# Optimization experiments

Measured on AMD Instinct MI355X. Metric: run time of the kernel, lower is better.

The kernel has to match this reference:

```python
import jax, jax.numpy as jnp
import numpy as np

GROUPS = 32
EPS = 1e-5


def group_norm(x, gamma, beta):
    # x: [B, C, H, W]; normalize over (C//G, H, W) within each of G groups
    B, C, H, W = x.shape
    xg = x.reshape(B, GROUPS, C // GROUPS, H, W)
    mean = xg.mean(axis=(2, 3, 4), keepdims=True)
    var = xg.var(axis=(2, 3, 4), keepdims=True)
    xg = (xg - mean) * jax.lax.rsqrt(var + EPS)
    x = xg.reshape(B, C, H, W)
    return x * gamma[None, :, None, None] + beta[None, :, None, None]


def conv1x1(x, W, b):
    # 1x1 conv == pointwise linear over channels. x: [B,C,H,W], W: [Cout,Cin]
    return jnp.einsum('oc,bchw->bohw', W, x) + b[None, :, None, None]


def setup_inputs() -> dict:
    key = jax.random.key(0)
    ks = jax.random.split(key, 6)
    B, C, H, W = 16, 512, 32, 32
    scale = 1.0 / np.sqrt(C)  # ~kaiming-ish init for 1x1 convs
    return {
        'x': jax.random.normal(ks[0], (B, C, H, W), jnp.float32),
        'gn_gamma': jnp.ones((C,), jnp.float32),
        'gn_beta': jnp.zeros((C,), jnp.float32),
        'Wq': jax.random.normal(ks[1], (C, C), jnp.float32) * scale,
        'bq': jnp.zeros((C,), jnp.float32),
        'Wk': jax.random.normal(ks[2], (C, C), jnp.float32) * scale,
        'bk': jnp.zeros((C,), jnp.float32),
        'Wv': jax.random.normal(ks[3], (C, C), jnp.float32) * scale,
        'bv': jnp.zeros((C,), jnp.float32),
        'Wp': jax.random.normal(ks[4], (C, C), jnp.float32) * scale,
        'bp': jnp.zeros((C,), jnp.float32),
    }


def reference(x, gn_gamma, gn_beta, Wq, bq, Wk, bk, Wv, bv, Wp, bp):
    B, C, H, W = x.shape
    h = group_norm(x, gn_gamma, gn_beta)
    q = conv1x1(h, Wq, bq).reshape(B, C, H * W)  # [B,C,T]
    k = conv1x1(h, Wk, bk).reshape(B, C, H * W)
    v = conv1x1(h, Wv, bv).reshape(B, C, H * W)
    # scores [B, T(query), S(key)] = q^T k, scaled by C^{-1/2}
    w = jnp.einsum('bct,bcs->bts', q, k) * (C ** -0.5)
    w = jax.nn.softmax(w, axis=-1)
    h = jnp.einsum('bts,bcs->bct', w, v).reshape(B, C, H, W)
    h = conv1x1(h, Wp, bp)
    return x + h
```

## Files before the change

kernel.cpp:

```cpp
#include <hip/hip_runtime.h>

typedef unsigned short u16;
typedef __bf16 bf16x8 __attribute__((ext_vector_type(8)));
typedef float f32x4 __attribute__((ext_vector_type(4)));

__device__ __forceinline__ u16 f2bf(float f) {
    unsigned u = __builtin_bit_cast(unsigned, f);
    u += 0x7fffu + ((u >> 16) & 1u);
    return (u16)(u >> 16);
}

#define GLDS16(g, l) __builtin_amdgcn_global_load_lds( \
    (const __attribute__((address_space(1))) void*)(g), \
    (__attribute__((address_space(3))) void*)(l), 16, 0, 0)

#define QK_SCALE 0.044194173824159216f

__global__ __launch_bounds__(256) void convert_kernel(
    const float* __restrict__ Wq, const float* __restrict__ Wk,
    const float* __restrict__ Wv, const float* __restrict__ Wp,
    const float* __restrict__ bq, const float* __restrict__ bk,
    const float* __restrict__ bv,
    u16* __restrict__ Wqkv, u16* __restrict__ Wpb, float* __restrict__ bqkv)
{
    int idx = blockIdx.x * 256 + threadIdx.x;
    if (idx < 786432) {
        int which = idx >> 18;
        int off   = idx & 262143;
        if (which == 0)
            Wqkv[idx] = f2bf(Wq[off] * QK_SCALE);
        else
            Wqkv[idx] = f2bf(((which == 1) ? Wk : Wv)[off]);
    } else {
        int off = idx - 786432;
        Wpb[off] = f2bf(Wp[off]);
    }
    if (idx < 1536) {
        float bvv = (idx < 512) ? bq[idx] * QK_SCALE
                  : (idx < 1024) ? bk[idx & 511] : bv[idx & 511];
        bqkv[idx] = bvv;
    }
}

__global__ __launch_bounds__(256) void gn_stats(
    const float* __restrict__ x, float2* __restrict__ stats)
{
    const int g = blockIdx.x, b = blockIdx.y, tid = threadIdx.x;
    const float* xg = x + ((size_t)b * 512 + (size_t)g * 16) * 1024;

    float s = 0.f, s2 = 0.f;
    const float4* x4 = (const float4*)xg;
    #pragma unroll 4
    for (int i = tid; i < 4096; i += 256) {
        float4 v = x4[i];
        s  += v.x + v.y + v.z + v.w;
        s2 += v.x * v.x + v.y * v.y + v.z * v.z + v.w * v.w;
    }
    #pragma unroll
    for (int off = 32; off; off >>= 1) {
        s  += __shfl_down(s, off);
        s2 += __shfl_down(s2, off);
    }
    __shared__ float rs[4], rs2[4];
    const int w = tid >> 6;
    if ((tid & 63) == 0) { rs[w] = s; rs2[w] = s2; }
    __syncthreads();
    if (tid == 0) {
        float S  = rs[0] + rs[1] + rs[2] + rs[3];
        float S2 = rs2[0] + rs2[1] + rs2[2] + rs2[3];
        float mean = S * (1.f / 16384.f);
        float var  = S2 * (1.f / 16384.f) - mean * mean;
        stats[b * 32 + g] = make_float2(mean, rsqrtf(var + 1e-5f));
    }
}

__global__ __launch_bounds__(256) void gn_apply(
    const float* __restrict__ x, const float* __restrict__ gamma,
    const float* __restrict__ beta, const float2* __restrict__ stats,
    u16* __restrict__ ht)
{
    const int tc = blockIdx.x, b = blockIdx.y, tid = threadIdx.x;
    const int t0 = tc * 32;

    __shared__ float2 st[32];
    __shared__ float ga[512], be[512];
    __shared__ __align__(16) u16 tile[512 * 32];

    if (tid < 32) st[tid] = stats[b * 32 + tid];
    for (int c = tid; c < 512; c += 256) { ga[c] = gamma[c]; be[c] = beta[c]; }
    __syncthreads();

    #pragma unroll
    for (int pass = 0; pass < 16; pass++) {
        const int c = pass * 32 + (tid >> 3);
        const int f = tid & 7;
        float4 v = *(const float4*)(x + ((size_t)(b * 512 + c)) * 1024 + t0 + f * 4);
        float2 s = st[c >> 4];
        float sc = s.y * ga[c];
        float sh = be[c] - s.x * sc;
        ushort4 hv = {f2bf(v.x * sc + sh), f2bf(v.y * sc + sh),
                      f2bf(v.z * sc + sh), f2bf(v.w * sc + sh)};
        const int slot = f ^ (c & 7) ^ ((c >> 3) & 7);
        *(ushort4*)(tile + c * 32 + slot * 4) = hv;
    }
    __syncthreads();

    #pragma unroll
    for (int p = 0; p < 8; p++) {
        const int t = p * 4 + (tid >> 6);
        const int l = tid & 63;
        u16 tmp[8];
        #pragma unroll
        for (int e = 0; e < 8; e++) {
            const int c = l * 8 + e;
            const int slot = (t >> 2) ^ (c & 7) ^ ((c >> 3) & 7);
            tmp[e] = tile[c * 32 + slot * 4 + (t & 3)];
        }
        *(uint4*)(ht + ((size_t)b * 1024 + t0 + t) * 512 + l * 8) = *(uint4*)tmp;
    }
}

__global__ __launch_bounds__(256) void softmax_kernel(u16* __restrict__ scores)
{
    const int row  = blockIdx.x * 4 + (threadIdx.x >> 6);
    const int lane = threadIdx.x & 63;
    u16* p = scores + (size_t)row * 1024 + lane * 16;

    uint4 w0 = ((const uint4*)p)[0];
    uint4 w1 = ((const uint4*)p)[1];
    unsigned wd[8] = {w0.x, w0.y, w0.z, w0.w, w1.x, w1.y, w1.z, w1.w};
    float v[16];
    #pragma unroll
    for (int i = 0; i < 8; i++) {
        v[2 * i]     = __builtin_bit_cast(float, wd[i] << 16);
        v[2 * i + 1] = __builtin_bit_cast(float, wd[i] & 0xffff0000u);
    }
    float m = v[0];
    #pragma unroll
    for (int i = 1; i < 16; i++) m = fmaxf(m, v[i]);
    #pragma unroll
    for (int off = 1; off < 64; off <<= 1) m = fmaxf(m, __shfl_xor(m, off));

    float s = 0.f;
    #pragma unroll
    for (int i = 0; i < 16; i++) { v[i] = __expf(v[i] - m); s += v[i]; }
    #pragma unroll
    for (int off = 1; off < 64; off <<= 1) s += __shfl_xor(s, off);
    const float inv = 1.0f / s;

    #pragma unroll
    for (int i = 0; i < 8; i++) {
        unsigned lo = f2bf(v[2 * i] * inv);
        unsigned hi = f2bf(v[2 * i + 1] * inv);
        wd[i] = lo | (hi << 16);
    }
    ((uint4*)p)[0] = make_uint4(wd[0], wd[1], wd[2], wd[3]);
    ((uint4*)p)[1] = make_uint4(wd[4], wd[5], wd[6], wd[7]);
}

template <int MODE>
__global__ __launch_bounds__(512, 2) void gemm_big(
    const u16* __restrict__ A, const u16* __restrict__ B,
    size_t strideA, size_t strideB, int lda, int ldb, int K,
    u16* __restrict__ o0, u16* __restrict__ o1, u16* __restrict__ o2,
    float* __restrict__ fo, const float* __restrict__ bias,
    const float* __restrict__ xres)
{
    __shared__ __align__(16) u16 smem[73728];
    u16* As = smem;
    u16* Bs = smem + 49152;

    const int tid  = threadIdx.x;
    const int lane = tid & 63;
    const int wave = tid >> 6;
    const int wm   = (wave & 3) * 64;
    const int wn   = (wave >> 2) * 64;

    const int gx = gridDim.x, gy = gridDim.y;
    int f = blockIdx.x + gx * (blockIdx.y + gy * blockIdx.z);
    const int nwg = gx * gy * (int)gridDim.z;
    f = (f & 7) * (nwg >> 3) + (f >> 3);
    const int bx  = f % gx;
    const int byz = f / gx;
    const int by  = byz % gy;
    const int b   = byz / gy;

    const u16* Ab = A + (size_t)b * strideA + (size_t)by * 256 * lda;
    const u16* Bb = B + (size_t)b * strideB + (size_t)bx * 128 * ldb;

    const int srow = tid >> 3;
    const int sc   = tid & 7;
    const int scg  = sc ^ (srow & 7);

    const u16* aSrc[4]; int aDst[4];
    #pragma unroll
    for (int u = 0; u < 4; u++) {
        aSrc[u] = Ab + (size_t)(u * 64 + srow) * lda + scg * 8;
        aDst[u] = (u * 64 + srow) * 64 + sc * 8;
    }
    const u16* bSrc[2]; int bDst[2];
    #pragma unroll
    for (int u = 0; u < 2; u++) {
        bSrc[u] = Bb + (size_t)(u * 64 + srow) * ldb + scg * 8;
        bDst[u] = (u * 64 + srow) * 64 + sc * 8;
    }

#define STAGEBIG(ko, sb) do { \
    _Pragma("unroll") \
    for (int u = 0; u < 4; u++) \
        GLDS16(aSrc[u] + (ko), As + (sb) * 16384 + aDst[u]); \
    _Pragma("unroll") \
    for (int u = 0; u < 2; u++) \
        GLDS16(bSrc[u] + (ko), Bs + (sb) * 8192 + bDst[u]); \
} while (0)

    const int l15 = lane & 15, lh = lane >> 4, rx = lane & 7;
    int aOff[4][2], bOff[4][2];
    #pragma unroll
    for (int i = 0; i < 4; i++)
        #pragma unroll
        for (int ks = 0; ks < 2; ks++) {
            const int slot = ((ks << 2) + lh) ^ rx;
            aOff[i][ks] = (wm + i * 16 + l15) * 64 + slot * 8;
            bOff[i][ks] = (wn + i * 16 + l15) * 64 + slot * 8;
        }

    f32x4 acc[4][4] = {};
    const int NT = K >> 6;

    STAGEBIG(0, 0);
    STAGEBIG(64, 1);

    int cbuf = 0, sbuf = 2;
    for (int t = 0; t < NT; ++t) {
        if (t == NT - 1) asm volatile("s_waitcnt vmcnt(0)" ::: "memory");
        else             asm volatile("s_waitcnt vmcnt(6)" ::: "memory");
        __builtin_amdgcn_s_barrier();
        __builtin_amdgcn_sched_barrier(0);

        if (t + 2 < NT) STAGEBIG((t + 2) * 64, sbuf);
        __builtin_amdgcn_sched_barrier(0);

        const u16* Ac = As + cbuf * 16384;
        const u16* Bc = Bs + cbuf * 8192;
        bf16x8 af[4][2], bf[4][2];
        #pragma unroll
        for (int i = 0; i < 4; i++)
            #pragma unroll
            for (int ks = 0; ks < 2; ks++) {
                af[i][ks] = *(const bf16x8*)(Ac + aOff[i][ks]);
                bf[i][ks] = *(const bf16x8*)(Bc + bOff[i][ks]);
            }

        __builtin_amdgcn_s_setprio(1);
        #pragma unroll
        for (int ks = 0; ks < 2; ks++)
            #pragma unroll
            for (int mi = 0; mi < 4; mi++)
                #pragma unroll
                for (int nj = 0; nj < 4; nj++)
                    acc[mi][nj] = __builtin_amdgcn_mfma_f32_16x16x32_bf16(
                        af[mi][ks], bf[nj][ks], acc[mi][nj], 0, 0, 0);
        __builtin_amdgcn_s_setprio(0);

        cbuf = (cbuf == 2) ? 0 : cbuf + 1;
        sbuf = (sbuf == 2) ? 0 : sbuf + 1;
    }
#undef STAGEBIG

    const int N0 = bx * 128;
    const int M0 = by * 256;

    __syncthreads();

    if (MODE != 3) {
        #pragma unroll
        for (int mi = 0; mi < 4; mi++) {
            const int mq = wm + mi * 16 + lh * 4;
            #pragma unroll
            for (int nj = 0; nj < 4; nj++) {
                const int n = wn + nj * 16 + l15;
                float bv = 0.f;
                if (MODE == 0) bv = bias[N0 + n];
                ushort4 hv = {f2bf(acc[mi][nj][0] + bv), f2bf(acc[mi][nj][1] + bv),
                              f2bf(acc[mi][nj][2] + bv), f2bf(acc[mi][nj][3] + bv)};
                *(ushort4*)((char*)smem + n * 512 +
                            ((((mq >> 3) ^ (n & 31))) << 4) + ((mq >> 2) & 1) * 8) = hv;
            }
        }
        __syncthreads();

        if (MODE == 0 && N0 < 1024) {
            #pragma unroll
            for (int p = 0; p < 8; p++) {
                const int m  = p * 32 + (tid >> 4);
                const int ci = tid & 15;
                u16 tmp[8];
                #pragma unroll
                for (int e = 0; e < 8; e++) {
                    const int n = ci * 8 + e;
                    tmp[e] = *(const u16*)((char*)smem + n * 512 +
                             (((m >> 3) ^ (n & 31)) << 4) + (m & 7) * 2);
                }
                u16* dst = (N0 < 512) ? o0 : o1;
                const int nn = (N0 & 511) + ci * 8;
                *(uint4*)(dst + ((size_t)b * 1024 + M0 + m) * 512 + nn) = *(uint4*)tmp;
            }
        } else {
            #pragma unroll
            for (int p = 0; p < 8; p++) {
                const int n  = p * 16 + (tid >> 5);
                const int gi = tid & 31;
                uint4 v4 = *(const uint4*)((char*)smem + n * 512 +
                                           ((gi ^ (n & 31)) << 4));
                u16* dst;
                if (MODE == 0)      dst = o2 + ((size_t)b * 512 + (N0 - 1024) + n) * 1024 + M0;
                else if (MODE == 1) dst = o0 + ((size_t)b * 1024 + N0 + n) * 1024 + M0;
                else                dst = o0 + ((size_t)b * 1024 + N0 + n) * 512 + M0;
                *(uint4*)(dst + gi * 8) = v4;
            }
        }
    } else {
        float* smf = (float*)smem;
        #pragma unroll
        for (int mi = 0; mi < 4; mi++) {
            const int mq = wm + mi * 16 + lh * 4;
            #pragma unroll
            for (int nj = 0; nj < 4; nj++) {
                const int n = wn + nj * 16 + l15;
                float4 v4 = {acc[mi][nj][0], acc[mi][nj][1],
                             acc[mi][nj][2], acc[mi][nj][3]};
                *(float4*)((char*)smf + n * 1024 +
                           (((mq >> 2) ^ (n & 63)) << 4)) = v4;
            }
        }
        __syncthreads();
        #pragma unroll
        for (int p = 0; p < 16; p++) {
            const int n  = p * 8 + (tid >> 6);
            const int gi = tid & 63;
            float4 v4 = *(const float4*)((char*)smf + n * 1024 +
                                         ((gi ^ (n & 63)) << 4));
            const size_t off = ((size_t)b * 512 + N0 + n) * 1024 + M0 + gi * 4;
            const float bv = bias[N0 + n];
            const float4 xv = *(const float4*)(xres + off);
            float4 ov = {v4.x + bv + xv.x, v4.y + bv + xv.y,
                         v4.z + bv + xv.z, v4.w + bv + xv.w};
            *(float4*)(fo + off) = ov;
        }
    }
}

extern "C" void kernel_launch(void* const* d_in, const int* in_sizes, int n_in,
                              void* d_out, int out_size, void* d_ws, size_t ws_size,
                              hipStream_t stream)
{
    const float* x     = (const float*)d_in[0];
    const float* gamma = (const float*)d_in[1];
    const float* beta  = (const float*)d_in[2];
    const float* Wq    = (const float*)d_in[3];
    const float* bq    = (const float*)d_in[4];
    const float* Wk    = (const float*)d_in[5];
    const float* bk    = (const float*)d_in[6];
    const float* Wv    = (const float*)d_in[7];
    const float* bv    = (const float*)d_in[8];
    const float* Wp    = (const float*)d_in[9];
    const float* bp    = (const float*)d_in[10];

    char* ws = (char*)d_ws;
    u16*   Wqkv   = (u16*)(ws + 0);
    u16*   Wpb    = (u16*)(ws + 1572864);
    float* bqkv   = (float*)(ws + 2097152);
    u16*   ht     = (u16*)(ws + 2105344);
    u16*   kt     = (u16*)(ws + 18882560);
    u16*   vv     = (u16*)(ws + 35659776);
    u16*   scores = (u16*)(ws + 52436992);
    u16*   qt  = (u16*)d_out;
    float2* stats = (float2*)((char*)d_out + 16777216);
    u16*   h2  = ht;
    float* out = (float*)d_out;

    convert_kernel<<<4096, 256, 0, stream>>>(Wq, Wk, Wv, Wp, bq, bk, bv,
                                             Wqkv, Wpb, bqkv);
    gn_stats<<<dim3(32, 16), 256, 0, stream>>>(x, stats);
    gn_apply<<<dim3(32, 16), 256, 0, stream>>>(x, gamma, beta, stats, ht);

    gemm_big<0><<<dim3(12, 4, 16), 512, 0, stream>>>(
        ht, Wqkv, 524288, 0, 512, 512, 512,
        qt, kt, vv, nullptr, bqkv, nullptr);

    gemm_big<1><<<dim3(8, 4, 16), 512, 0, stream>>>(
        kt, qt, 524288, 524288, 512, 512, 512,
        scores, nullptr, nullptr, nullptr, nullptr, nullptr);

    softmax_kernel<<<4096, 256, 0, stream>>>(scores);

    gemm_big<2><<<dim3(8, 2, 16), 512, 0, stream>>>(
        vv, scores, 524288, 1048576, 1024, 1024, 1024,
        h2, nullptr, nullptr, nullptr, nullptr, nullptr);

    gemm_big<3><<<dim3(4, 4, 16), 512, 0, stream>>>(
        h2, Wpb, 524288, 0, 512, 512, 512,
        nullptr, nullptr, nullptr, out, bp, x);
}
```

Baseline: 241.2 us.

## Fuse softmax into score GEMM epilogue with deferred row normalization

Removes the standalone softmax kernel. The score GEMM now writes exp(score) without max subtraction and atomically adds per-row sums into a zeroed buffer. The PV GEMM divides by those sums in its epilogue. The main loop also splits the prefetch into two halves interleaved with the MFMA k-steps, and the Q/K projection stores directly from registers instead of going through an LDS transpose. Skipping the max subtraction risks overflow for large scores, the atomics add contention, and the direct stores are scattered 2-byte writes.

New measurement: 222.1 us. -7.9%, faster.

```diff
diff --git a/kernel.cpp b/kernel.cpp
--- a/kernel.cpp
+++ b/kernel.cpp
@@ -21,7 +21,8 @@
     const float* __restrict__ Wv, const float* __restrict__ Wp,
     const float* __restrict__ bq, const float* __restrict__ bk,
     const float* __restrict__ bv,
-    u16* __restrict__ Wqkv, u16* __restrict__ Wpb, float* __restrict__ bqkv)
+    u16* __restrict__ Wqkv, u16* __restrict__ Wpb, float* __restrict__ bqkv,
+    float* __restrict__ rsum)
 {
     int idx = blockIdx.x * 256 + threadIdx.x;
     if (idx < 786432) {
@@ -40,6 +41,7 @@
                   : (idx < 1024) ? bk[idx & 511] : bv[idx & 511];
         bqkv[idx] = bvv;
     }
+    if (idx < 16384) rsum[idx] = 0.f;
 }
 
 __global__ __launch_bounds__(256) void gn_stats(
@@ -120,46 +122,8 @@
     }
 }
 
-__global__ __launch_bounds__(256) void softmax_kernel(u16* __restrict__ scores)
-{
-    const int row  = blockIdx.x * 4 + (threadIdx.x >> 6);
-    const int lane = threadIdx.x & 63;
-    u16* p = scores + (size_t)row * 1024 + lane * 16;
-
-    uint4 w0 = ((const uint4*)p)[0];
-    uint4 w1 = ((const uint4*)p)[1];
-    unsigned wd[8] = {w0.x, w0.y, w0.z, w0.w, w1.x, w1.y, w1.z, w1.w};
-    float v[16];
-    #pragma unroll
-    for (int i = 0; i < 8; i++) {
-        v[2 * i]     = __builtin_bit_cast(float, wd[i] << 16);
-        v[2 * i + 1] = __builtin_bit_cast(float, wd[i] & 0xffff0000u);
-    }
-    float m = v[0];
-    #pragma unroll
-    for (int i = 1; i < 16; i++) m = fmaxf(m, v[i]);
-    #pragma unroll
-    for (int off = 1; off < 64; off <<= 1) m = fmaxf(m, __shfl_xor(m, off));
-
-    float s = 0.f;
-    #pragma unroll
-    for (int i = 0; i < 16; i++) { v[i] = __expf(v[i] - m); s += v[i]; }
-    #pragma unroll
-    for (int off = 1; off < 64; off <<= 1) s += __shfl_xor(s, off);
-    const float inv = 1.0f / s;
-
-    #pragma unroll
-    for (int i = 0; i < 8; i++) {
-        unsigned lo = f2bf(v[2 * i] * inv);
-        unsigned hi = f2bf(v[2 * i + 1] * inv);
-        wd[i] = lo | (hi << 16);
-    }
-    ((uint4*)p)[0] = make_uint4(wd[0], wd[1], wd[2], wd[3]);
-    ((uint4*)p)[1] = make_uint4(wd[4], wd[5], wd[6], wd[7]);
-}
-
 template <int MODE>
-__global__ __launch_bounds__(512, 2) void gemm_big(
+__global__ __launch_bounds__(512, 2) void gemm_nt(
     const u16* __restrict__ A, const u16* __restrict__ B,
     size_t strideA, size_t strideB, int lda, int ldb, int K,
     u16* __restrict__ o0, u16* __restrict__ o1, u16* __restrict__ o2,
@@ -205,15 +169,6 @@
         bDst[u] = (u * 64 + srow) * 64 + sc * 8;
     }
 
-#define STAGEBIG(ko, sb) do { \
-    _Pragma("unroll") \
-    for (int u = 0; u < 4; u++) \
-        GLDS16(aSrc[u] + (ko), As + (sb) * 16384 + aDst[u]); \
-    _Pragma("unroll") \
-    for (int u = 0; u < 2; u++) \
-        GLDS16(bSrc[u] + (ko), Bs + (sb) * 8192 + bDst[u]); \
-} while (0)
-
     const int l15 = lane & 15, lh = lane >> 4, rx = lane & 7;
     int aOff[4][2], bOff[4][2];
     #pragma unroll
@@ -228,99 +183,156 @@
     f32x4 acc[4][4] = {};
     const int NT = K >> 6;
 
-    STAGEBIG(0, 0);
-    STAGEBIG(64, 1);
+    #pragma unroll
+    for (int u = 0; u < 4; u++) GLDS16(aSrc[u], As + aDst[u]);
+    #pragma unroll
+    for (int u = 0; u < 2; u++) GLDS16(bSrc[u], Bs + bDst[u]);
+    #pragma unroll
+    for (int u = 0; u < 4; u++) GLDS16(aSrc[u] + 64, As + 16384 + aDst[u]);
+    #pragma unroll
+    for (int u = 0; u < 2; u++) GLDS16(bSrc[u] + 64, Bs + 8192 + bDst[u]);
 
     int cbuf = 0, sbuf = 2;
     for (int t = 0; t < NT; ++t) {
         if (t == NT - 1) asm volatile("s_waitcnt vmcnt(0)" ::: "memory");
         else             asm volatile("s_waitcnt vmcnt(6)" ::: "memory");
         __builtin_amdgcn_s_barrier();
-        __builtin_amdgcn_sched_barrier(0);
-
-        if (t + 2 < NT) STAGEBIG((t + 2) * 64, sbuf);
-        __builtin_amdgcn_sched_barrier(0);
 
         const u16* Ac = As + cbuf * 16384;
         const u16* Bc = Bs + cbuf * 8192;
-        bf16x8 af[4][2], bf[4][2];
-        #pragma unroll
-        for (int i = 0; i < 4; i++)
-            #pragma unroll
-            for (int ks = 0; ks < 2; ks++) {
-                af[i][ks] = *(const bf16x8*)(Ac + aOff[i][ks]);
-                bf[i][ks] = *(const bf16x8*)(Bc + bOff[i][ks]);
-            }
-
-        __builtin_amdgcn_s_setprio(1);
-        #pragma unroll
-        for (int ks = 0; ks < 2; ks++)
+        u16* Asb = As + sbuf * 16384;
+        u16* Bsb = Bs + sbuf * 8192;
+        const int ko = (t + 2) * 64;
+        const bool pf = (t + 2 < NT);
+
+        if (pf) {
+            GLDS16(aSrc[0] + ko, Asb + aDst[0]);
+            GLDS16(aSrc[1] + ko, Asb + aDst[1]);
+            GLDS16(bSrc[0] + ko, Bsb + bDst[0]);
+        }
+        {
+            bf16x8 af[4], bfr[4];
+            #pragma unroll
+            for (int i = 0; i < 4; i++) {
+                af[i]  = *(const bf16x8*)(Ac + aOff[i][0]);
+                bfr[i] = *(const bf16x8*)(Bc + bOff[i][0]);
+            }
+            __builtin_amdgcn_s_setprio(1);
             #pragma unroll
             for (int mi = 0; mi < 4; mi++)
                 #pragma unroll
                 for (int nj = 0; nj < 4; nj++)
                     acc[mi][nj] = __builtin_amdgcn_mfma_f32_16x16x32_bf16(
-                        af[mi][ks], bf[nj][ks], acc[mi][nj], 0, 0, 0);
-        __builtin_amdgcn_s_setprio(0);
+                        af[mi], bfr[nj], acc[mi][nj], 0, 0, 0);
+            __builtin_amdgcn_s_setprio(0);
+        }
+        if (pf) {
+            GLDS16(aSrc[2] + ko, Asb + aDst[2]);
+            GLDS16(aSrc[3] + ko, Asb + aDst[3]);
+            GLDS16(bSrc[1] + ko, Bsb + bDst[1]);
+        }
+        {
+            bf16x8 af[4], bfr[4];
+            #pragma unroll
+            for (int i = 0; i < 4; i++) {
+                af[i]  = *(const bf16x8*)(Ac + aOff[i][1]);
+                bfr[i] = *(const bf16x8*)(Bc + bOff[i][1]);
+            }
+            __builtin_amdgcn_s_setprio(1);
+            #pragma unroll
+            for (int mi = 0; mi < 4; mi++)
+                #pragma unroll
+                for (int nj = 0; nj < 4; nj++)
+                    acc[mi][nj] = __builtin_amdgcn_mfma_f32_16x16x32_bf16(
+                        af[mi], bfr[nj], acc[mi][nj], 0, 0, 0);
+            __builtin_amdgcn_s_setprio(0);
+        }
 
         cbuf = (cbuf == 2) ? 0 : cbuf + 1;
         sbuf = (sbuf == 2) ? 0 : sbuf + 1;
     }
-#undef STAGEBIG
 
     const int N0 = bx * 128;
     const int M0 = by * 256;
 
-    __syncthreads();
-
-    if (MODE != 3) {
+    if (MODE == 0 && N0 < 1024) {
+        u16* dst = (N0 < 512) ? o0 : o1;
+        const int nn0 = N0 & 511;
+        #pragma unroll
+        for (int nj = 0; nj < 4; nj++) {
+            const int n = wn + nj * 16 + l15;
+            const float bv = bias[N0 + n];
+            #pragma unroll
+            for (int mi = 0; mi < 4; mi++) {
+                const int mq = M0 + wm + mi * 16 + lh * 4;
+                const size_t base = ((size_t)b * 1024 + mq) * 512 + nn0 + n;
+                dst[base]        = f2bf(acc[mi][nj][0] + bv);
+                dst[base + 512]  = f2bf(acc[mi][nj][1] + bv);
+                dst[base + 1024] = f2bf(acc[mi][nj][2] + bv);
+                dst[base + 1536] = f2bf(acc[mi][nj][3] + bv);
+            }
+        }
+    } else if (MODE != 3) {
+        __syncthreads();
+        float rinv_[4];
+        if (MODE == 2) {
+            #pragma unroll
+            for (int nj = 0; nj < 4; nj++)
+                rinv_[nj] = 1.0f / xres[(size_t)b * 1024 + N0 + wn + nj * 16 + l15];
+        }
         #pragma unroll
         for (int mi = 0; mi < 4; mi++) {
             const int mq = wm + mi * 16 + lh * 4;
             #pragma unroll
             for (int nj = 0; nj < 4; nj++) {
                 const int n = wn + nj * 16 + l15;
-                float bv = 0.f;
-                if (MODE == 0) bv = bias[N0 + n];
-                ushort4 hv = {f2bf(acc[mi][nj][0] + bv), f2bf(acc[mi][nj][1] + bv),
-                              f2bf(acc[mi][nj][2] + bv), f2bf(acc[mi][nj][3] + bv)};
+                float a0 = acc[mi][nj][0], a1 = acc[mi][nj][1];
+                float a2 = acc[mi][nj][2], a3 = acc[mi][nj][3];
+                if (MODE == 0) {
+                    const float bv = bias[N0 + n];
+                    a0 += bv; a1 += bv; a2 += bv; a3 += bv;
+                }
+                if (MODE == 1) {
+                    a0 = __expf(a0); a1 = __expf(a1);
+                    a2 = __expf(a2); a3 = __expf(a3);
+                }
+                if (MODE == 2) {
+                    a0 *= rinv_[nj]; a1 *= rinv_[nj];
+                    a2 *= rinv_[nj]; a3 *= rinv_[nj];
+                }
+                ushort4 hv = {f2bf(a0), f2bf(a1), f2bf(a2), f2bf(a3)};
                 *(ushort4*)((char*)smem + n * 512 +
-                            ((((mq >> 3) ^ (n & 31))) << 4) + ((mq >> 2) & 1) * 8) = hv;
+                            (((mq >> 3) ^ (n & 31)) << 4) + ((mq >> 2) & 1) * 8) = hv;
             }
         }
         __syncthreads();
-
-        if (MODE == 0 && N0 < 1024) {
-            #pragma unroll
-            for (int p = 0; p < 8; p++) {
-                const int m  = p * 32 + (tid >> 4);
-                const int ci = tid & 15;
-                u16 tmp[8];
+        #pragma unroll
+        for (int p = 0; p < 8; p++) {
+            const int n  = p * 16 + (tid >> 5);
+            const int gi = tid & 31;
+            uint4 v4 = *(const uint4*)((char*)smem + n * 512 +
+                                       ((gi ^ (n & 31)) << 4));
+            u16* dst;
+            if (MODE == 0)      dst = o2 + ((size_t)b * 512 + (N0 - 1024) + n) * 1024 + M0;
+            else if (MODE == 1) dst = o0 + ((size_t)b * 1024 + N0 + n) * 1024 + M0;
+            else                dst = o0 + ((size_t)b * 1024 + N0 + n) * 512 + M0;
+            *(uint4*)(dst + gi * 8) = v4;
+            if (MODE == 1) {
+                unsigned wd_[4] = {v4.x, v4.y, v4.z, v4.w};
+                float rsm = 0.f;
                 #pragma unroll
-                for (int e = 0; e < 8; e++) {
-                    const int n = ci * 8 + e;
-                    tmp[e] = *(const u16*)((char*)smem + n * 512 +
-                             (((m >> 3) ^ (n & 31)) << 4) + (m & 7) * 2);
-                }
-                u16* dst = (N0 < 512) ? o0 : o1;
-                const int nn = (N0 & 511) + ci * 8;
-                *(uint4*)(dst + ((size_t)b * 1024 + M0 + m) * 512 + nn) = *(uint4*)tmp;
-            }
-        } else {
-            #pragma unroll
-            for (int p = 0; p < 8; p++) {
-                const int n  = p * 16 + (tid >> 5);
-                const int gi = tid & 31;
-                uint4 v4 = *(const uint4*)((char*)smem + n * 512 +
-                                           ((gi ^ (n & 31)) << 4));
-                u16* dst;
-                if (MODE == 0)      dst = o2 + ((size_t)b * 512 + (N0 - 1024) + n) * 1024 + M0;
-                else if (MODE == 1) dst = o0 + ((size_t)b * 1024 + N0 + n) * 1024 + M0;
-                else                dst = o0 + ((size_t)b * 1024 + N0 + n) * 512 + M0;
-                *(uint4*)(dst + gi * 8) = v4;
+                for (int q = 0; q < 4; q++)
+                    rsm += __builtin_bit_cast(float, wd_[q] << 16)
+                         + __builtin_bit_cast(float, wd_[q] & 0xffff0000u);
+                #pragma unroll
+                for (int off = 1; off < 32; off <<= 1)
+                    rsm += __shfl_xor(rsm, off);
+                if (gi == 0)
+                    atomicAdd(fo + ((size_t)b * 1024 + N0 + n), rsm);
             }
         }
     } else {
+        __syncthreads();
         float* smf = (float*)smem;
         #pragma unroll
         for (int mi = 0; mi < 4; mi++) {
@@ -377,29 +389,28 @@
     u16*   scores = (u16*)(ws + 52436992);
     u16*   qt  = (u16*)d_out;
     float2* stats = (float2*)((char*)d_out + 16777216);
+    float* rsum   = (float*)((char*)d_out + 16781312);
     u16*   h2  = ht;
     float* out = (float*)d_out;
 
     convert_kernel<<<4096, 256, 0, stream>>>(Wq, Wk, Wv, Wp, bq, bk, bv,
-                                             Wqkv, Wpb, bqkv);
+                                             Wqkv, Wpb, bqkv, rsum);
     gn_stats<<<dim3(32, 16), 256, 0, stream>>>(x, stats);
     gn_apply<<<dim3(32, 16), 256, 0, stream>>>(x, gamma, beta, stats, ht);
 
-    gemm_big<0><<<dim3(12, 4, 16), 512, 0, stream>>>(
+    gemm_nt<0><<<dim3(12, 4, 16), 512, 0, stream>>>(
         ht, Wqkv, 524288, 0, 512, 512, 512,
         qt, kt, vv, nullptr, bqkv, nullptr);
 
-    gemm_big<1><<<dim3(8, 4, 16), 512, 0, stream>>>(
+    gemm_nt<1><<<dim3(8, 4, 16), 512, 0, stream>>>(
         kt, qt, 524288, 524288, 512, 512, 512,
-        scores, nullptr, nullptr, nullptr, nullptr, nullptr);
-
-    softmax_kernel<<<4096, 256, 0, stream>>>(scores);
-
-    gemm_big<2><<<dim3(8, 2, 16), 512, 0, stream>>>(
+        scores, nullptr, nullptr, rsum, nullptr, nullptr);
+
+    gemm_nt<2><<<dim3(8, 2, 16), 512, 0, stream>>>(
         vv, scores, 524288, 1048576, 1024, 1024, 1024,
-        h2, nullptr, nullptr, nullptr, nullptr, nullptr);
-
-    gemm_big<3><<<dim3(4, 4, 16), 512, 0, stream>>>(
+        h2, nullptr, nullptr, nullptr, nullptr, rsum);
+
+    gemm_nt<3><<<dim3(4, 4, 16), 512, 0, stream>>>(
         h2, Wpb, 524288, 0, 512, 512, 512,
         nullptr, nullptr, nullptr, out, bp, x);
 }
```
